# Optimization experiments

Hardware: AMD Instinct MI355X
Metric: run time of the kernel (lower is better)

The kernel has to match this reference:

```python
import jax, jax.numpy as jnp
import numpy as np

N_HEAD = 8
D_MODEL = 128  # per-head dim == d_model in this 'interpretable' MHA
B, S = 2, 2048
LN_EPS = 1e-3  # keras LayerNormalization default epsilon


def setup_inputs() -> dict:
    key = jax.random.key(0)
    ks = jax.random.split(key, 8)
    sc = 1.0 / np.sqrt(D_MODEL)
    q = jax.random.normal(ks[0], (B, S, D_MODEL), jnp.float32)
    k = jax.random.normal(ks[1], (B, S, D_MODEL), jnp.float32)
    v = jax.random.normal(ks[2], (B, S, D_MODEL), jnp.float32)
    # multiplicative causal mask (lower-triangular ones), broadcast over B,H
    mask = jnp.tril(jnp.ones((S, S), jnp.float32))[None, None, :, :]
    Wq = jax.random.normal(ks[3], (D_MODEL, N_HEAD * D_MODEL), jnp.float32) * sc
    Wk = jax.random.normal(ks[4], (D_MODEL, N_HEAD * D_MODEL), jnp.float32) * sc
    Wv = jax.random.normal(ks[5], (D_MODEL, N_HEAD * D_MODEL), jnp.float32) * sc
    Wo = jax.random.normal(ks[6], (N_HEAD * D_MODEL, D_MODEL), jnp.float32) * sc
    gamma = jnp.ones((D_MODEL,), jnp.float32)
    beta = jnp.zeros((D_MODEL,), jnp.float32)
    return {"q": q, "k": k, "v": v, "mask": mask, "Wq": Wq, "Wk": Wk,
            "Wv": Wv, "Wo": Wo, "gamma": gamma, "beta": beta}


def reference(q, k, v, mask, Wq, Wk, Wv, Wo, gamma, beta):
    b = q.shape[0]
    # projections -> [B, H, S, D]
    def split_heads(x):
        return x.reshape(b, -1, N_HEAD, D_MODEL).transpose(0, 2, 1, 3)
    qs = split_heads(q @ Wq)
    ks_ = split_heads(k @ Wk)
    vs = split_heads(v @ Wv)
    scores = jnp.einsum('bhqd,bhkd->bhqk', qs, ks_) / jnp.sqrt(jnp.float32(D_MODEL))
    scores = scores * mask  # multiplicative mask (NOT additive -inf)
    attn = jax.nn.softmax(scores, axis=-1)
    # dropout layers are identity at inference
    out = jnp.einsum('bhqk,bhkd->bhqd', attn, vs)
    out = out.transpose(0, 2, 1, 3).reshape(b, -1, N_HEAD * D_MODEL)
    out = out @ Wo
    # keras LayerNorm (axis=-1, eps=1e-3)
    mu = jnp.mean(out, axis=-1, keepdims=True)
    var = jnp.var(out, axis=-1, keepdims=True)
    out = (out - mu) * jax.lax.rsqrt(var + LN_EPS) * gamma + beta
    return out
```

## Files before the change

kernel.cpp:

```cpp
#include <hip/hip_runtime.h>
#include <math.h>

#define B 2
#define S 2048
#define H 8
#define D 128
#define DM 1024
#define BH 16

typedef unsigned short u16;
typedef __attribute__((ext_vector_type(8))) short bf16x8;
typedef __attribute__((ext_vector_type(8))) unsigned short u16x8;
typedef __attribute__((ext_vector_type(4))) float f32x4;

__device__ __forceinline__ float bf2f(u16 x) {
    union { unsigned u; float f; } c; c.u = ((unsigned)x) << 16; return c.f;
}
__device__ __forceinline__ u16 f2bf(float f) {
    union { unsigned u; float f; } c; c.f = f;
    unsigned u = c.u; u += 0x7fffu + ((u >> 16) & 1u);
    return (u16)(u >> 16);
}
__device__ __forceinline__ u16 ftr(float f) {
    union { unsigned u; float f; } c; c.f = f;
    return (u16)(c.u >> 16);
}

#define MFMA16(a, b, c) __builtin_amdgcn_mfma_f32_16x16x32_bf16((a), (b), (c), 0, 0, 0)

__global__ __launch_bounds__(256) void prep_kernel(
    const float* __restrict__ Wq, const float* __restrict__ Wk, const float* __restrict__ Wv,
    const float* __restrict__ Wo, u16* __restrict__ WT, u16* __restrict__ WoT)
{
    __shared__ __align__(16) u16 Wl[128][132];
    int tid = threadIdx.x, by = blockIdx.x;
    if (by < 16) {
        int k0 = by * 64;
#pragma unroll
        for (int i = 0; i < 8; i++) {
            int e = i * 256 + tid; int kk = e >> 5, n4 = e & 31;
            float4 w4 = *(const float4*)&Wo[(size_t)(k0 + kk) * D + n4 * 4];
            ushort4 p; p.x = ftr(w4.x); p.y = ftr(w4.y); p.z = ftr(w4.z); p.w = ftr(w4.w);
            *(ushort4*)&Wl[kk][n4 * 4] = p;
        }
        __syncthreads();
#pragma unroll
        for (int i = 0; i < 4; i++) {
            int e = i * 256 + tid; int n = e >> 3, ko = e & 7;
            u16x8 g;
#pragma unroll
            for (int j = 0; j < 8; j++) g[j] = Wl[ko * 8 + j][n];
            *(u16x8*)&WoT[(size_t)n * DM + k0 + ko * 8] = g;
        }
    } else {
        int tile = by - 16;
        int t = tile >> 3, h = tile & 7;
        const float* W = (t == 0) ? Wq : (t == 1) ? Wk : Wv;
        int col0 = h * 128;
#pragma unroll
        for (int i = 0; i < 16; i++) {
            int e = i * 256 + tid; int kk = e >> 5, n4 = e & 31;
            float4 w4 = *(const float4*)&W[(size_t)kk * DM + col0 + n4 * 4];
            ushort4 p; p.x = ftr(w4.x); p.y = ftr(w4.y); p.z = ftr(w4.z); p.w = ftr(w4.w);
            *(ushort4*)&Wl[kk][n4 * 4] = p;
        }
        __syncthreads();
        u16* WTt = WT + (size_t)tile * (128 * 128);
#pragma unroll
        for (int i = 0; i < 8; i++) {
            int e = i * 256 + tid; int n = e >> 4, ko = e & 15;
            u16x8 g;
#pragma unroll
            for (int j = 0; j < 8; j++) g[j] = Wl[ko * 8 + j][n];
            *(u16x8*)&WTt[(size_t)n * 128 + ko * 8] = g;
        }
    }
}

__global__ __launch_bounds__(256) void proj_kernel(
    const float* __restrict__ q, const float* __restrict__ k, const float* __restrict__ v,
    const u16* __restrict__ WT,
    u16* __restrict__ Qo, u16* __restrict__ Ko, u16* __restrict__ VTo,
    float* __restrict__ Csum)
{
    __shared__ __align__(16) u16 Xs[64][136];
    __shared__ __align__(16) u16 Ws[128][136];
    int tid = threadIdx.x;
    int m0 = blockIdx.x * 64;
    int by = blockIdx.y;
    int t = by >> 3;
    int h = by & 7;
    const float* X = (t == 0) ? q : (t == 1) ? k : v;
    const u16* WTt = WT + (size_t)(t * 8 + h) * (128 * 128);

#pragma unroll
    for (int i = 0; i < 8; i++) {
        int e = i * 256 + tid; int r = e >> 5, c4 = e & 31;
        float4 x4 = *(const float4*)&X[(size_t)(m0 + r) * D + c4 * 4];
        ushort4 p; p.x = ftr(x4.x); p.y = ftr(x4.y); p.z = ftr(x4.z); p.w = ftr(x4.w);
        *(ushort4*)&Xs[r][c4 * 4] = p;
    }
#pragma unroll
    for (int i = 0; i < 8; i++) {
        int e = i * 256 + tid; int n = e >> 4, c8 = e & 15;
        *(u16x8*)&Ws[n][c8 * 8] = *(const u16x8*)&WTt[(size_t)n * 128 + c8 * 8];
    }
    __syncthreads();

    int w = tid >> 6, lane = tid & 63, quad = lane >> 4, ln = lane & 15;
    bf16x8 aX[4];
#pragma unroll
    for (int ks = 0; ks < 4; ks++)
        aX[ks] = *(const bf16x8*)&Xs[w * 16 + ln][ks * 32 + quad * 8];

    f32x4 zero = {0.f, 0.f, 0.f, 0.f};
    f32x4 acc[8];
#pragma unroll
    for (int nt = 0; nt < 8; nt++) acc[nt] = zero;

#pragma unroll
    for (int ks = 0; ks < 4; ks++) {
        bf16x8 bW[8];
#pragma unroll
        for (int nt = 0; nt < 8; nt++)
            bW[nt] = *(const bf16x8*)&Ws[nt * 16 + ln][ks * 32 + quad * 8];
#pragma unroll
        for (int nt = 0; nt < 8; nt++)
            acc[nt] = MFMA16(aX[ks], bW[nt], acc[nt]);
    }

    int bb = m0 >> 11, ss0 = m0 & 2047;
    int bh = bb * 8 + h;
    __syncthreads();
    if (t < 2) {
        u16 (*Ct)[136] = Xs;
        u16* O = (t == 0) ? Qo : Ko;
#pragma unroll
        for (int nt = 0; nt < 8; nt++)
#pragma unroll
            for (int r = 0; r < 4; r++)
                Ct[w * 16 + quad * 4 + r][nt * 16 + ln] = f2bf(acc[nt][r]);
        __syncthreads();
#pragma unroll
        for (int i = 0; i < 4; i++) {
            int e = i * 256 + tid; int r = e >> 4, c8 = e & 15;
            *(u16x8*)&O[((size_t)bh * S + ss0 + r) * D + c8 * 8] = *(const u16x8*)&Ct[r][c8 * 8];
        }
    } else {
        u16 (*Ct)[68] = (u16 (*)[68])&Xs[0][0];
#pragma unroll
        for (int nt = 0; nt < 8; nt++)
#pragma unroll
            for (int r = 0; r < 4; r++)
                Ct[nt * 16 + ln][w * 16 + quad * 4 + r] = f2bf(acc[nt][r]);
        __syncthreads();
#pragma unroll
        for (int i = 0; i < 4; i++) {
            int e = i * 256 + tid; int dloc = e >> 3, c8 = e & 7;
            *(u16x8*)&VTo[((size_t)bh * D + dloc) * S + ss0 + c8 * 8] =
                *(const u16x8*)&Ct[dloc][c8 * 8];
        }
        if (tid < 128) {
            int d = tid;
            float s = 0.f;
#pragma unroll
            for (int i = 0; i < 8; i++) {
                u16x8 v8 = *(const u16x8*)&Ct[d][i * 8];
#pragma unroll
                for (int j = 0; j < 8; j++) s += bf2f(v8[j]);
            }
            Csum[((size_t)bh * 32 + (ss0 >> 6)) * D + d] = s;
        }
    }
}

__global__ __launch_bounds__(512, 4) void attn_kernel(
    const u16* __restrict__ Qb, const u16* __restrict__ Kb, const u16* __restrict__ VTg,
    const float* __restrict__ Csum, u16* __restrict__ HOb)
{
    __shared__ __align__(16) u16 Qs[64][132];
    __shared__ __align__(16) u16 Ps[2][64][132];
    __shared__ float Lred[4][64];

    int tid = threadIdx.x;
    int bh = blockIdx.x;
    int y  = blockIdx.y;
    int qb = 31 - y;
    int q0 = qb * 64;
    int ntile = (qb >> 1) + 1;
    int w = tid >> 6, lane = tid & 63, quad = lane >> 4, ln = lane & 15;
    const u16* Qp  = Qb  + (size_t)bh * S * D;
    const u16* Kp  = Kb  + (size_t)bh * S * D;
    const u16* VTp = VTg + (size_t)bh * D * S;

#pragma unroll
    for (int i = 0; i < 2; i++) {
        int e = i * 512 + tid; int r = e >> 4, c8 = e & 15;
        *(u16x8*)&Qs[r][c8 * 8] = *(const u16x8*)&Qp[(size_t)(q0 + r) * D + c8 * 8];
    }
    const u16* krow = &Kp[(size_t)(w * 16 + ln) * D + quad * 8];
    const u16* vrow = &VTp[(size_t)(w * 16 + ln) * S + quad * 8];
    bf16x8 kfrag[4];
#pragma unroll
    for (int ks = 0; ks < 4; ks++)
        kfrag[ks] = *(const bf16x8*)&krow[ks * 32];
    __syncthreads();

    f32x4 zero = {0.f, 0.f, 0.f, 0.f};
    f32x4 accPV[4], acc_l[4];
#pragma unroll
    for (int rf = 0; rf < 4; rf++) { accPV[rf] = zero; acc_l[rf] = zero; }
    bf16x8 bOnes;
#pragma unroll
    for (int j = 0; j < 8; j++) bOnes[j] = (short)0x3F80;
    const float scale = 0.08838834764831845f;

    int p = 0;
    for (int kt = 0; kt < ntile; kt++) {
        int k0 = kt * 128;
        bool pf = (kt + 1 < ntile);
        bf16x8 vb[4];
#pragma unroll
        for (int ks = 0; ks < 4; ks++)
            vb[ks] = *(const bf16x8*)&vrow[k0 + ks * 32];
        bf16x8 kn[4];
        if (pf) {
#pragma unroll
            for (int ks = 0; ks < 4; ks++)
                kn[ks] = *(const bf16x8*)&krow[(size_t)(k0 + 128) * D + ks * 32];
        }
        f32x4 s[4];
#pragma unroll
        for (int rf = 0; rf < 4; rf++) s[rf] = zero;
        __builtin_amdgcn_s_setprio(1);
#pragma unroll
        for (int ks = 0; ks < 4; ks++) {
#pragma unroll
            for (int rf = 0; rf < 4; rf++) {
                bf16x8 aQ = *(const bf16x8*)&Qs[rf * 16 + ln][ks * 32 + quad * 8];
                s[rf] = MFMA16(aQ, kfrag[ks], s[rf]);
            }
        }
        __builtin_amdgcn_s_setprio(0);
        int colb = k0 + w * 16 + ln;
#pragma unroll
        for (int rf = 0; rf < 4; rf++) {
            int rowb = q0 + rf * 16 + quad * 4;
#pragma unroll
            for (int r = 0; r < 4; r++) {
                float tv = (colb <= rowb + r) ? s[rf][r] : 0.f;
                Ps[p][rf * 16 + quad * 4 + r][w * 16 + ln] = f2bf(__expf(tv * scale));
            }
        }
        __syncthreads();
        __builtin_amdgcn_s_setprio(1);
#pragma unroll
        for (int ks = 0; ks < 4; ks++) {
            bf16x8 aP[4];
#pragma unroll
            for (int rf = 0; rf < 4; rf++)
                aP[rf] = *(const bf16x8*)&Ps[p][rf * 16 + ln][ks * 32 + quad * 8];
            if (w < 4 && ks == w) {
#pragma unroll
                for (int rf = 0; rf < 4; rf++) acc_l[rf] = MFMA16(aP[rf], bOnes, acc_l[rf]);
            }
#pragma unroll
            for (int rf = 0; rf < 4; rf++)
                accPV[rf] = MFMA16(aP[rf], vb[ks], accPV[rf]);
        }
        __builtin_amdgcn_s_setprio(0);
        if (pf) {
#pragma unroll
            for (int ks = 0; ks < 4; ks++) kfrag[ks] = kn[ks];
        }
        p ^= 1;
    }

    if (w < 4 && ln == 0) {
#pragma unroll
        for (int rf = 0; rf < 4; rf++)
#pragma unroll
            for (int r = 0; r < 4; r++)
                Lred[w][rf * 16 + quad * 4 + r] = acc_l[rf][r];
    }
    __syncthreads();

    int nt64 = 2 * ntile;
    float suf = 0.f;
    for (int c = 31; c >= nt64; c--)
        suf += Csum[((size_t)(bh * 32 + c)) * D + w * 16 + ln];
    int scount = S - ntile * 128;
    int b = bh >> 3, h = bh & 7;
#pragma unroll
    for (int rf = 0; rf < 4; rf++)
#pragma unroll
        for (int r = 0; r < 4; r++) {
            int row = rf * 16 + quad * 4 + r;
            int srow = q0 + row;
            float l = Lred[0][row] + Lred[1][row] + Lred[2][row] + Lred[3][row]
                      + (float)scount;
            float inv = 1.f / l;
            HOb[((size_t)(b * S + srow)) * DM + h * D + w * 16 + ln] =
                f2bf((accPV[rf][r] + suf) * inv);
        }
}

__global__ __launch_bounds__(256) void out_ln_kernel(
    const u16* __restrict__ HOb, const u16* __restrict__ WoT,
    const float* __restrict__ gamma, const float* __restrict__ beta,
    float* __restrict__ out)
{
    __shared__ __align__(16) u16 HOs[16][1048];
    __shared__ float Cs[16][132];
    int tid = threadIdx.x;
    int m0 = blockIdx.x * 16;
    int w = tid >> 6, lane = tid & 63, quad = lane >> 4, ln = lane & 15;
#pragma unroll
    for (int i = 0; i < 8; i++) {
        int e = i * 256 + tid; int r = e >> 7, c8 = e & 127;
        *(u16x8*)&HOs[r][c8 * 8] = *(const u16x8*)&HOb[(size_t)(m0 + r) * DM + c8 * 8];
    }
    __syncthreads();
    f32x4 zero = {0.f, 0.f, 0.f, 0.f};
    f32x4 acc[2] = {zero, zero};
#pragma unroll 4
    for (int ks = 0; ks < 32; ks++) {
        bf16x8 aH = *(const bf16x8*)&HOs[ln][ks * 32 + quad * 8];
        bf16x8 w0 = *(const bf16x8*)&WoT[(size_t)(w * 32 + ln) * DM + ks * 32 + quad * 8];
        bf16x8 w1 = *(const bf16x8*)&WoT[(size_t)(w * 32 + 16 + ln) * DM + ks * 32 + quad * 8];
        acc[0] = MFMA16(aH, w0, acc[0]);
        acc[1] = MFMA16(aH, w1, acc[1]);
    }
#pragma unroll
    for (int ct = 0; ct < 2; ct++)
#pragma unroll
        for (int r = 0; r < 4; r++)
            Cs[quad * 4 + r][w * 32 + ct * 16 + ln] = acc[ct][r];
    __syncthreads();

    int row = tid >> 4, t16 = tid & 15;
    float xv[8], sum = 0.f, sq = 0.f;
#pragma unroll
    for (int j = 0; j < 8; j++) {
        float x = Cs[row][t16 * 8 + j];
        xv[j] = x; sum += x; sq += x * x;
    }
#pragma unroll
    for (int off = 1; off < 16; off <<= 1) {
        sum += __shfl_xor(sum, off);
        sq  += __shfl_xor(sq, off);
    }
    float mu = sum * (1.f / 128.f);
    float var = sq * (1.f / 128.f) - mu * mu;
    float rstd = rsqrtf(var + 1e-3f);
    float o[8];
#pragma unroll
    for (int j = 0; j < 8; j++) {
        int c = t16 * 8 + j;
        o[j] = (xv[j] - mu) * rstd * gamma[c] + beta[c];
    }
    float* op = &out[(size_t)(m0 + row) * D + t16 * 8];
    *(float4*)&op[0] = *(float4*)&o[0];
    *(float4*)&op[4] = *(float4*)&o[4];
}

extern "C" void kernel_launch(void* const* d_in, const int* in_sizes, int n_in,
                              void* d_out, int out_size, void* d_ws, size_t ws_size,
                              hipStream_t stream)
{
    const float* q     = (const float*)d_in[0];
    const float* k     = (const float*)d_in[1];
    const float* v     = (const float*)d_in[2];
    const float* Wq    = (const float*)d_in[4];
    const float* Wk    = (const float*)d_in[5];
    const float* Wv    = (const float*)d_in[6];
    const float* Wo    = (const float*)d_in[7];
    const float* gamma = (const float*)d_in[8];
    const float* beta  = (const float*)d_in[9];

    u16* ws16 = (u16*)d_ws;
    u16* Qb  = ws16;
    u16* Kb  = ws16 + 4194304;
    u16* VT  = ws16 + 8388608;
    u16* HOb = ws16 + 12582912;
    u16* WoT = ws16 + 16777216;
    u16* WT  = ws16 + 16908288;
    float* Csum = (float*)((char*)d_ws + 35651584);

    prep_kernel<<<40, 256, 0, stream>>>(Wq, Wk, Wv, Wo, WT, WoT);
    proj_kernel<<<dim3(64, 24), 256, 0, stream>>>(q, k, v, WT, Qb, Kb, VT, Csum);
    attn_kernel<<<dim3(BH, 32), 512, 0, stream>>>(Qb, Kb, VT, Csum, HOb);
    out_ln_kernel<<<256, 256, 0, stream>>>(HOb, WoT, gamma, beta, (float*)d_out);
}
```

Measured before the change: 165.6 us.

## Stage K and V tiles through double-buffered LDS with coalesced loads

Replaces the per-lane strided global fragment loads of K and V^T with cooperative, coalesced 16-byte loads into double-buffered LDS tiles, staged through registers for the next tile. Q fragments are hoisted into registers once, reusing a V buffer slot for the initial Q staging. The P buffer is reduced to a single buffer and an extra barrier is added per tile. LDS use grows to about 150KB and launch bounds drop to 2 blocks per SM, which lowers occupancy.

After: 157.6 us. 1.05x faster.

```diff
diff --git a/kernel.cpp b/kernel.cpp
--- a/kernel.cpp
+++ b/kernel.cpp
@@ -174,12 +174,13 @@
     }
 }
 
-__global__ __launch_bounds__(512, 4) void attn_kernel(
+__global__ __launch_bounds__(512, 2) void attn_kernel(
     const u16* __restrict__ Qb, const u16* __restrict__ Kb, const u16* __restrict__ VTg,
     const float* __restrict__ Csum, u16* __restrict__ HOb)
 {
-    __shared__ __align__(16) u16 Qs[64][132];
-    __shared__ __align__(16) u16 Ps[2][64][132];
+    __shared__ __align__(16) u16 Ks[2][128][132];
+    __shared__ __align__(16) u16 Vt[2][128][132];
+    __shared__ __align__(16) u16 Ps[64][132];
     __shared__ float Lred[4][64];
 
     int tid = threadIdx.x;
@@ -196,15 +197,25 @@
 #pragma unroll
     for (int i = 0; i < 2; i++) {
         int e = i * 512 + tid; int r = e >> 4, c8 = e & 15;
-        *(u16x8*)&Qs[r][c8 * 8] = *(const u16x8*)&Qp[(size_t)(q0 + r) * D + c8 * 8];
-    }
-    const u16* krow = &Kp[(size_t)(w * 16 + ln) * D + quad * 8];
-    const u16* vrow = &VTp[(size_t)(w * 16 + ln) * S + quad * 8];
-    bf16x8 kfrag[4];
-#pragma unroll
-    for (int ks = 0; ks < 4; ks++)
-        kfrag[ks] = *(const bf16x8*)&krow[ks * 32];
-    __syncthreads();
+        *(u16x8*)&Vt[1][r][c8 * 8] = *(const u16x8*)&Qp[(size_t)(q0 + r) * D + c8 * 8];
+    }
+#pragma unroll
+    for (int i = 0; i < 4; i++) {
+        int e = i * 512 + tid; int r = e >> 4, c8 = e & 15;
+        *(u16x8*)&Ks[0][r][c8 * 8] = *(const u16x8*)&Kp[(size_t)r * D + c8 * 8];
+    }
+#pragma unroll
+    for (int i = 0; i < 4; i++) {
+        int e = i * 512 + tid; int dd = e >> 4, c8 = e & 15;
+        *(u16x8*)&Vt[0][dd][c8 * 8] = *(const u16x8*)&VTp[(size_t)dd * S + c8 * 8];
+    }
+    __syncthreads();
+    bf16x8 aQ[4][4];
+#pragma unroll
+    for (int rf = 0; rf < 4; rf++)
+#pragma unroll
+        for (int ks = 0; ks < 4; ks++)
+            aQ[rf][ks] = *(const bf16x8*)&Vt[1][rf * 16 + ln][ks * 32 + quad * 8];
 
     f32x4 zero = {0.f, 0.f, 0.f, 0.f};
     f32x4 accPV[4], acc_l[4];
@@ -215,19 +226,22 @@
     for (int j = 0; j < 8; j++) bOnes[j] = (short)0x3F80;
     const float scale = 0.08838834764831845f;
 
-    int p = 0;
     for (int kt = 0; kt < ntile; kt++) {
+        int cur = kt & 1, nxt = cur ^ 1;
         int k0 = kt * 128;
         bool pf = (kt + 1 < ntile);
-        bf16x8 vb[4];
-#pragma unroll
-        for (int ks = 0; ks < 4; ks++)
-            vb[ks] = *(const bf16x8*)&vrow[k0 + ks * 32];
-        bf16x8 kn[4];
+        u16x8 kreg[4], vreg[4];
         if (pf) {
 #pragma unroll
-            for (int ks = 0; ks < 4; ks++)
-                kn[ks] = *(const bf16x8*)&krow[(size_t)(k0 + 128) * D + ks * 32];
+            for (int i = 0; i < 4; i++) {
+                int e = i * 512 + tid; int r = e >> 4, c8 = e & 15;
+                kreg[i] = *(const u16x8*)&Kp[(size_t)(k0 + 128 + r) * D + c8 * 8];
+            }
+#pragma unroll
+            for (int i = 0; i < 4; i++) {
+                int e = i * 512 + tid; int dd = e >> 4, c8 = e & 15;
+                vreg[i] = *(const u16x8*)&VTp[(size_t)dd * S + k0 + 128 + c8 * 8];
+            }
         }
         f32x4 s[4];
 #pragma unroll
@@ -235,11 +249,10 @@
         __builtin_amdgcn_s_setprio(1);
 #pragma unroll
         for (int ks = 0; ks < 4; ks++) {
-#pragma unroll
-            for (int rf = 0; rf < 4; rf++) {
-                bf16x8 aQ = *(const bf16x8*)&Qs[rf * 16 + ln][ks * 32 + quad * 8];
-                s[rf] = MFMA16(aQ, kfrag[ks], s[rf]);
-            }
+            bf16x8 bK = *(const bf16x8*)&Ks[cur][w * 16 + ln][ks * 32 + quad * 8];
+#pragma unroll
+            for (int rf = 0; rf < 4; rf++)
+                s[rf] = MFMA16(aQ[rf][ks], bK, s[rf]);
         }
         __builtin_amdgcn_s_setprio(0);
         int colb = k0 + w * 16 + ln;
@@ -249,7 +262,7 @@
 #pragma unroll
             for (int r = 0; r < 4; r++) {
                 float tv = (colb <= rowb + r) ? s[rf][r] : 0.f;
-                Ps[p][rf * 16 + quad * 4 + r][w * 16 + ln] = f2bf(__expf(tv * scale));
+                Ps[rf * 16 + quad * 4 + r][w * 16 + ln] = f2bf(__expf(tv * scale));
             }
         }
         __syncthreads();
@@ -259,21 +272,30 @@
             bf16x8 aP[4];
 #pragma unroll
             for (int rf = 0; rf < 4; rf++)
-                aP[rf] = *(const bf16x8*)&Ps[p][rf * 16 + ln][ks * 32 + quad * 8];
+                aP[rf] = *(const bf16x8*)&Ps[rf * 16 + ln][ks * 32 + quad * 8];
+            bf16x8 vb = *(const bf16x8*)&Vt[cur][w * 16 + ln][ks * 32 + quad * 8];
             if (w < 4 && ks == w) {
 #pragma unroll
                 for (int rf = 0; rf < 4; rf++) acc_l[rf] = MFMA16(aP[rf], bOnes, acc_l[rf]);
             }
 #pragma unroll
             for (int rf = 0; rf < 4; rf++)
-                accPV[rf] = MFMA16(aP[rf], vb[ks], accPV[rf]);
+                accPV[rf] = MFMA16(aP[rf], vb, accPV[rf]);
         }
         __builtin_amdgcn_s_setprio(0);
         if (pf) {
 #pragma unroll
-            for (int ks = 0; ks < 4; ks++) kfrag[ks] = kn[ks];
-        }
-        p ^= 1;
+            for (int i = 0; i < 4; i++) {
+                int e = i * 512 + tid; int r = e >> 4, c8 = e & 15;
+                *(u16x8*)&Ks[nxt][r][c8 * 8] = kreg[i];
+            }
+#pragma unroll
+            for (int i = 0; i < 4; i++) {
+                int e = i * 512 + tid; int dd = e >> 4, c8 = e & 15;
+                *(u16x8*)&Vt[nxt][dd][c8 * 8] = vreg[i];
+            }
+        }
+        __syncthreads();
     }
 
     if (w < 4 && ln == 0) {
```
